# Kernel optimization log

Hardware: AMD Instinct MI355X
Metric: run time of the kernel (lower is better)

Reference implementation:

```python
import jax, jax.numpy as jnp
import numpy as np

DIM = 2048
INTER = 1408
N_EXPERTS = 16
TOP_K = 2
N_SHARED = 2
SHARED_INTER = N_SHARED * INTER  # 2816


def setup_inputs() -> dict:
    key = jax.random.key(0)
    ks = jax.random.split(key, 9)
    s = 0.02
    return {
        "x": jax.random.normal(ks[0], (4, 2048, DIM), dtype=jnp.float32),
        "gate_w": jax.random.normal(ks[1], (N_EXPERTS, DIM), dtype=jnp.float32) * s,
        "w1": jax.random.normal(ks[2], (N_EXPERTS, INTER, DIM), dtype=jnp.float32) * s,
        "w2": jax.random.normal(ks[3], (N_EXPERTS, DIM, INTER), dtype=jnp.float32) * s,
        "w3": jax.random.normal(ks[4], (N_EXPERTS, INTER, DIM), dtype=jnp.float32) * s,
        "sw1": jax.random.normal(ks[5], (SHARED_INTER, DIM), dtype=jnp.float32) * s,
        "sw2": jax.random.normal(ks[6], (DIM, SHARED_INTER), dtype=jnp.float32) * s,
        "sw3": jax.random.normal(ks[7], (SHARED_INTER, DIM), dtype=jnp.float32) * s,
    }


def _swiglu(t, wa, wb, wo):
    # t: [T, d_in]; wa, wb: [d_h, d_in]; wo: [d_out, d_h]
    h = jax.nn.silu(t @ wa.T) * (t @ wb.T)
    return h @ wo.T


def reference(x, gate_w, w1, w2, w3, sw1, sw2, sw3):
    shape = x.shape
    t = x.reshape(-1, DIM)                      # [T, dim]
    scores = jax.nn.softmax(t @ gate_w.T, axis=-1)  # [T, E]
    weights, indices = jax.lax.top_k(scores, TOP_K)  # [T, k] each

    y = jnp.zeros_like(t)
    # Small fixed loop over experts (structurally distinct weights).
    # Per-token combine weight for expert e: sum over top-k slots routed to e
    # (matches y[idx] += expert(x[idx]) * weights[idx, top]; zero weight for
    # unrouted tokens reproduces the counts[i]==0 skip exactly).
    for e in range(N_EXPERTS):
        w_e = jnp.sum(jnp.where(indices == e, weights, 0.0), axis=-1)  # [T]
        y = y + _swiglu(t, w1[e], w3[e], w2[e]) * w_e[:, None]

    z = _swiglu(t, sw1, sw3, sw2)               # shared experts MLP
    return (y + z).reshape(shape)
```

## Files before the change

kernel.cpp:

```cpp
#include <hip/hip_runtime.h>
#include <hip/hip_bf16.h>

#define DIM 2048
#define INTER 1408
#define NEXP 16
#define NTOK 8192
#define SINTER 2816

typedef __attribute__((ext_vector_type(8))) short bf16x8;
typedef __attribute__((ext_vector_type(4))) float f32x4;
typedef __attribute__((ext_vector_type(4))) unsigned short u16x4;
typedef __attribute__((ext_vector_type(8))) unsigned short u16x8;

#define VMCNT(n) asm volatile("s_waitcnt vmcnt(" #n ")" ::: "memory")
#define BARRIER() __builtin_amdgcn_s_barrier()

__device__ __forceinline__ unsigned short f2bf(float f) {
    union { float f; unsigned u; } a; a.f = f;
    unsigned r = a.u + 0x7fffu + ((a.u >> 16) & 1u);
    return (unsigned short)(r >> 16);
}

__device__ __forceinline__ void gload16(const void* g, void* lds) {
    __builtin_amdgcn_global_load_lds(
        (const __attribute__((address_space(1))) void*)g,
        (__attribute__((address_space(3))) void*)lds, 16, 0, 0);
}

__global__ __launch_bounds__(256) void cast_bf16(const float* __restrict__ s,
                                                 unsigned short* __restrict__ d,
                                                 long long n) {
    long long i = ((long long)blockIdx.x * 256 + threadIdx.x) * 8;
    if (i >= n) return;
    float4 a = *(const float4*)(s + i), b = *(const float4*)(s + i + 4);
    u16x8 o = { f2bf(a.x), f2bf(a.y), f2bf(a.z), f2bf(a.w),
                f2bf(b.x), f2bf(b.y), f2bf(b.z), f2bf(b.w) };
    *(u16x8*)(d + i) = o;
}

__global__ __launch_bounds__(256) void gate_topk(
    const float* __restrict__ x, const float* __restrict__ gw,
    unsigned short* __restrict__ xb,
    int* __restrict__ counts, int* __restrict__ toklist, float* __restrict__ tokw) {
    int wave = threadIdx.x >> 6;
    int lane = threadIdx.x & 63;
    int tok  = blockIdx.x * 4 + wave;
    const float* xr = x + (size_t)tok * DIM;
    unsigned short* xbr = xb + (size_t)tok * DIM;

    float part[NEXP];
#pragma unroll
    for (int e = 0; e < NEXP; ++e) part[e] = 0.f;
#pragma unroll
    for (int c = 0; c < DIM / 256; ++c) {
        float4 xv = *(const float4*)(xr + c * 256 + lane * 4);
        u16x4 xo = { f2bf(xv.x), f2bf(xv.y), f2bf(xv.z), f2bf(xv.w) };
        *(u16x4*)(xbr + c * 256 + lane * 4) = xo;
#pragma unroll
        for (int e = 0; e < NEXP; ++e) {
            float4 g = *(const float4*)(gw + e * DIM + c * 256 + lane * 4);
            part[e] += xv.x * g.x + xv.y * g.y + xv.z * g.z + xv.w * g.w;
        }
    }
#pragma unroll
    for (int e = 0; e < NEXP; ++e) {
        float v = part[e];
#pragma unroll
        for (int off = 32; off; off >>= 1) v += __shfl_xor(v, off);
        part[e] = v;
    }
    float mx = part[0];
#pragma unroll
    for (int e = 1; e < NEXP; ++e) mx = fmaxf(mx, part[e]);
    float Z = 0.f;
#pragma unroll
    for (int e = 0; e < NEXP; ++e) Z += expf(part[e] - mx);
    int i1 = 0; float m1 = part[0];
#pragma unroll
    for (int e = 1; e < NEXP; ++e) if (part[e] > m1) { m1 = part[e]; i1 = e; }
    int i2 = -1; float m2 = -1e30f;
#pragma unroll
    for (int e = 0; e < NEXP; ++e) if (e != i1 && part[e] > m2) { m2 = part[e]; i2 = e; }
    if (lane == 0) {
        float w1v = expf(m1 - mx) / Z;
        float w2v = expf(m2 - mx) / Z;
        int p1 = atomicAdd(&counts[i1], 1);
        toklist[i1 * NTOK + p1] = tok; tokw[i1 * NTOK + p1] = w1v;
        int p2 = atomicAdd(&counts[i2], 1);
        toklist[i2 * NTOK + p2] = tok; tokw[i2 * NTOK + p2] = w2v;
    }
}

__global__ void prefix_k(const int* __restrict__ counts, int* __restrict__ base) {
    if (threadIdx.x == 0) {
        int acc = 0;
        for (int e = 0; e < NEXP; ++e) { base[e] = acc; acc += counts[e]; }
        base[16] = acc;
        base[17] = acc + NTOK;
    }
}

__device__ __forceinline__ int swz(int r) { return (r ^ (r >> 2)) & 3; }

__global__ __launch_bounds__(512, 2) void gemm1(
    const unsigned short* __restrict__ xb,
    const unsigned short* __restrict__ w1b, const unsigned short* __restrict__ w3b,
    const unsigned short* __restrict__ sw1b, const unsigned short* __restrict__ sw3b,
    const int* __restrict__ counts, const int* __restrict__ base,
    const int* __restrict__ toklist, unsigned short* __restrict__ hbuf) {
    const int e   = blockIdx.z;
    const int cnt = (e < NEXP) ? counts[e] : NTOK;
    const int m0  = blockIdx.y * 256;
    if (m0 >= cnt) return;
    const int n0  = blockIdx.x * 128;
    const size_t woff = (size_t)((e < NEXP) ? e : e - NEXP) * INTER * DIM;
    const unsigned short* B1 = ((e < NEXP) ? w1b : sw1b) + woff;
    const unsigned short* B3 = ((e < NEXP) ? w3b : sw3b) + woff;
    const int hbase = base[e];
    const int* tl = toklist + e * NTOK;

    __shared__ __attribute__((aligned(16))) unsigned short As[4][8192];
    __shared__ __attribute__((aligned(16))) unsigned short B1s[4][4096];
    __shared__ __attribute__((aligned(16))) unsigned short B3s[4][4096];

    const int tid = threadIdx.x;
    const int w = tid >> 6, lu = tid & 63;
    const int wr = w >> 1, wc = w & 1;
    const int lr = lu & 15, hi = lu >> 4;

    const int row0 = tid >> 2, row1 = row0 + 128;
    const int c0 = (tid & 3) ^ swz(row0);
    int g0 = m0 + row0, g1 = m0 + row1;
    int t0, t1;
    if (e < NEXP) { t0 = (g0 < cnt) ? tl[g0] : 0; t1 = (g1 < cnt) ? tl[g1] : 0; }
    else          { t0 = g0; t1 = g1; }
    const unsigned short* aSrc0 = xb + (size_t)t0 * DIM + c0 * 8;
    const unsigned short* aSrc1 = xb + (size_t)t1 * DIM + c0 * 8;
    const unsigned short* b1Src = B1 + (size_t)(n0 + row0) * DIM + c0 * 8;
    const unsigned short* b3Src = B3 + (size_t)(n0 + row0) * DIM + c0 * 8;

    int aoff[4], boff[4];
#pragma unroll
    for (int m = 0; m < 4; ++m) {
        int r = wr * 64 + m * 16 + lr;
        aoff[m] = r * 64 + ((swz(r) ^ hi) << 4);
    }
#pragma unroll
    for (int n = 0; n < 4; ++n) {
        int r = wc * 64 + n * 16 + lr;
        boff[n] = r * 64 + ((swz(r) ^ hi) << 4);
    }

    f32x4 acc1[4][4], acc3[4][4];
#pragma unroll
    for (int m = 0; m < 4; ++m)
#pragma unroll
        for (int n = 0; n < 4; ++n) {
            acc1[m][n] = (f32x4){0.f, 0.f, 0.f, 0.f};
            acc3[m][n] = (f32x4){0.f, 0.f, 0.f, 0.f};
        }

    const int H = DIM / 32;

    auto STAGE = [&](int hh) {
        int hb = hh & 3;
        int kc = hh * 32;
        gload16(aSrc0 + kc, &As[hb][tid * 8]);
        gload16(aSrc1 + kc, &As[hb][4096 + tid * 8]);
        gload16(b1Src + kc, &B1s[hb][tid * 8]);
        gload16(b3Src + kc, &B3s[hb][tid * 8]);
    };

    STAGE(0); STAGE(1);
    VMCNT(4);
    BARRIER();

    for (int h = 0; h < H; ++h) {
        const int hb = h & 3;
        const char* As_ = (const char*)&As[hb][0];
        const char* B1_ = (const char*)&B1s[hb][0];
        const char* B3_ = (const char*)&B3s[hb][0];
        bf16x8 af[4], b1f[4], b3f[4];
#pragma unroll
        for (int m = 0; m < 4; ++m) af[m] = *(const bf16x8*)(As_ + aoff[m]);
#pragma unroll
        for (int n = 0; n < 4; ++n) {
            b1f[n] = *(const bf16x8*)(B1_ + boff[n]);
            b3f[n] = *(const bf16x8*)(B3_ + boff[n]);
        }
        if (h + 2 < H) { STAGE(h + 2); VMCNT(4); }
        else           { VMCNT(0); }
        BARRIER();
        __builtin_amdgcn_s_setprio(1);
#pragma unroll
        for (int n = 0; n < 4; ++n)
#pragma unroll
            for (int m = 0; m < 4; ++m)
                acc1[m][n] = __builtin_amdgcn_mfma_f32_16x16x32_bf16(af[m], b1f[n], acc1[m][n], 0, 0, 0);
#pragma unroll
        for (int n = 0; n < 4; ++n)
#pragma unroll
            for (int m = 0; m < 4; ++m)
                acc3[m][n] = __builtin_amdgcn_mfma_f32_16x16x32_bf16(af[m], b3f[n], acc3[m][n], 0, 0, 0);
        __builtin_amdgcn_s_setprio(0);
    }

#pragma unroll
    for (int m = 0; m < 4; ++m) {
#pragma unroll
        for (int i = 0; i < 4; ++i) {
            int row  = wr * 64 + m * 16 + hi * 4 + i;
            int grow = m0 + row;
            if (grow < cnt) {
                size_t ro = (size_t)(hbase + grow) * INTER;
#pragma unroll
                for (int n = 0; n < 4; ++n) {
                    int col = n0 + wc * 64 + n * 16 + lr;
                    float a = acc1[m][n][i];
                    float hv = a / (1.f + __expf(-a)) * acc3[m][n][i];
                    hbuf[ro + col] = f2bf(hv);
                }
            }
        }
    }
}

__global__ __launch_bounds__(512, 2) void gemm2(
    const unsigned short* __restrict__ hbuf,
    const unsigned short* __restrict__ w2b, const unsigned short* __restrict__ sw2b,
    const int* __restrict__ counts, const int* __restrict__ base,
    const int* __restrict__ toklist, const float* __restrict__ tokw,
    float* __restrict__ out) {
    const int e   = blockIdx.z;
    const int cnt = (e < NEXP) ? counts[e] : NTOK;
    const int m0  = blockIdx.y * 256;
    if (m0 >= cnt) return;
    const int n0  = blockIdx.x * 128;
    const int hbase = base[e];
    const size_t bstride = (e < NEXP) ? INTER : SINTER;
    const unsigned short* Bb = (e < NEXP) ? w2b + (size_t)e * DIM * INTER
                                          : sw2b + (size_t)(e - NEXP) * INTER;

    __shared__ __attribute__((aligned(16))) unsigned short Ah[4][8192];
    __shared__ __attribute__((aligned(16))) unsigned short Bh[4][4096];

    const int tid = threadIdx.x;
    const int w = tid >> 6, lu = tid & 63;
    const int wr = w >> 1, wc = w & 1;
    const int lr = lu & 15, hi = lu >> 4;

    const int row0 = tid >> 2, row1 = row0 + 128;
    const int c0 = (tid & 3) ^ swz(row0);
    const unsigned short* aSrc0 = hbuf + (size_t)(hbase + m0 + row0) * INTER + c0 * 8;
    const unsigned short* aSrc1 = hbuf + (size_t)(hbase + m0 + row1) * INTER + c0 * 8;
    const unsigned short* bSrc  = Bb + (size_t)(n0 + row0) * bstride + c0 * 8;

    int aoff[4], boff[4];
#pragma unroll
    for (int m = 0; m < 4; ++m) {
        int r = wr * 64 + m * 16 + lr;
        aoff[m] = r * 64 + ((swz(r) ^ hi) << 4);
    }
#pragma unroll
    for (int n = 0; n < 4; ++n) {
        int r = wc * 64 + n * 16 + lr;
        boff[n] = r * 64 + ((swz(r) ^ hi) << 4);
    }

    f32x4 acc[4][4];
#pragma unroll
    for (int m = 0; m < 4; ++m)
#pragma unroll
        for (int n = 0; n < 4; ++n) acc[m][n] = (f32x4){0.f, 0.f, 0.f, 0.f};

    const int H = INTER / 32;

    auto STAGE = [&](int hh) {
        int hb = hh & 3;
        int kc = hh * 32;
        gload16(aSrc0 + kc, &Ah[hb][tid * 8]);
        gload16(aSrc1 + kc, &Ah[hb][4096 + tid * 8]);
        gload16(bSrc  + kc, &Bh[hb][tid * 8]);
    };

    STAGE(0); STAGE(1);
    VMCNT(3);
    BARRIER();

    for (int h = 0; h < H; ++h) {
        const int hb = h & 3;
        const char* A_ = (const char*)&Ah[hb][0];
        const char* B_ = (const char*)&Bh[hb][0];
        bf16x8 af[4], bf[4];
#pragma unroll
        for (int m = 0; m < 4; ++m) af[m] = *(const bf16x8*)(A_ + aoff[m]);
#pragma unroll
        for (int n = 0; n < 4; ++n) bf[n] = *(const bf16x8*)(B_ + boff[n]);
        if (h + 2 < H) { STAGE(h + 2); VMCNT(3); }
        else           { VMCNT(0); }
        BARRIER();
        __builtin_amdgcn_s_setprio(1);
#pragma unroll
        for (int n = 0; n < 4; ++n)
#pragma unroll
            for (int m = 0; m < 4; ++m)
                acc[m][n] = __builtin_amdgcn_mfma_f32_16x16x32_bf16(af[m], bf[n], acc[m][n], 0, 0, 0);
        __builtin_amdgcn_s_setprio(0);
    }

#pragma unroll
    for (int m = 0; m < 4; ++m) {
#pragma unroll
        for (int i = 0; i < 4; ++i) {
            int row  = wr * 64 + m * 16 + hi * 4 + i;
            int grow = m0 + row;
            if (grow < cnt) {
                int tok; float wt;
                if (e < NEXP) { tok = toklist[e * NTOK + grow]; wt = tokw[e * NTOK + grow]; }
                else          { tok = grow; wt = 1.f; }
                float* orow = out + (size_t)tok * DIM + n0 + wc * 64 + lr;
#pragma unroll
                for (int n = 0; n < 4; ++n)
                    unsafeAtomicAdd(orow + n * 16, acc[m][n][i] * wt);
            }
        }
    }
}

extern "C" void kernel_launch(void* const* d_in, const int* in_sizes, int n_in,
                              void* d_out, int out_size, void* d_ws, size_t ws_size,
                              hipStream_t stream) {
    const float* x   = (const float*)d_in[0];
    const float* gw  = (const float*)d_in[1];
    const float* w1  = (const float*)d_in[2];
    const float* w2  = (const float*)d_in[3];
    const float* w3  = (const float*)d_in[4];
    const float* sw1 = (const float*)d_in[5];
    const float* sw2 = (const float*)d_in[6];
    const float* sw3 = (const float*)d_in[7];
    float* out = (float*)d_out;

    char* ws = (char*)d_ws;
    int*   counts  = (int*)ws;
    int*   basep   = (int*)(ws + 128);
    int*   toklist = (int*)(ws + 4096);
    float* tokw    = (float*)(ws + 4096 + (size_t)NEXP * NTOK * 4);
    unsigned short* hbuf = (unsigned short*)(ws + (2u << 20));

    const size_t hbytes = (size_t)4 * NTOK * INTER * 2;
    const size_t offx   = (2ull << 20) + hbytes;
    const size_t xbytes = (size_t)NTOK * DIM * 2;
    const size_t offw   = offx + xbytes;
    const size_t wB     = (size_t)NEXP * INTER * DIM * 2;
    const size_t swB    = (size_t)SINTER * DIM * 2;

    unsigned short* xb   = (unsigned short*)(ws + offx);
    unsigned short* w1b  = (unsigned short*)(ws + offw);
    unsigned short* w3b  = (unsigned short*)(ws + offw + wB);
    unsigned short* w2b  = (unsigned short*)(ws + offw + 2 * wB);
    unsigned short* sw1b = (unsigned short*)(ws + offw + 3 * wB);
    unsigned short* sw3b = (unsigned short*)(ws + offw + 3 * wB + swB);
    unsigned short* sw2b = (unsigned short*)(ws + offw + 3 * wB + 2 * swB);

    hipMemsetAsync(counts, 0, 64, stream);
    hipMemsetAsync(d_out, 0, (size_t)out_size * sizeof(float), stream);

    gate_topk<<<NTOK / 4, 256, 0, stream>>>(x, gw, xb, counts, toklist, tokw);
    prefix_k<<<1, 64, 0, stream>>>(counts, basep);

    auto cast = [&](const float* s, unsigned short* d, long long n) {
        cast_bf16<<<(int)((n / 8 + 255) / 256), 256, 0, stream>>>(s, d, n);
    };
    cast(w1, w1b, (long long)NEXP * INTER * DIM);
    cast(w3, w3b, (long long)NEXP * INTER * DIM);
    cast(sw1, sw1b, (long long)SINTER * DIM);
    cast(sw3, sw3b, (long long)SINTER * DIM);

    gemm1<<<dim3(INTER / 128, NTOK / 256, 18), 512, 0, stream>>>(
        xb, w1b, w3b, sw1b, sw3b, counts, basep, toklist, hbuf);

    cast(w2, w2b, (long long)NEXP * INTER * DIM);
    cast(sw2, sw2b, (long long)SINTER * DIM);

    gemm2<<<dim3(DIM / 128, NTOK / 256, 18), 512, 0, stream>>>(
        hbuf, w2b, sw2b, counts, basep, toklist, tokw, out);
}
```

Before: 1.345 ms.

## Replace atomic scatter-add output with bf16 staging buffer and combine kernel

```diff
diff --git a/kernel.cpp b/kernel.cpp
--- a/kernel.cpp
+++ b/kernel.cpp
@@ -19,6 +19,9 @@
     union { float f; unsigned u; } a; a.f = f;
     unsigned r = a.u + 0x7fffu + ((a.u >> 16) & 1u);
     return (unsigned short)(r >> 16);
+}
+__device__ __forceinline__ float bf2f(unsigned short u) {
+    union { unsigned u; float f; } a; a.u = ((unsigned)u) << 16; return a.f;
 }
 
 __device__ __forceinline__ void gload16(const void* g, void* lds) {
@@ -41,7 +44,8 @@
 __global__ __launch_bounds__(256) void gate_topk(
     const float* __restrict__ x, const float* __restrict__ gw,
     unsigned short* __restrict__ xb,
-    int* __restrict__ counts, int* __restrict__ toklist, float* __restrict__ tokw) {
+    int* __restrict__ counts, int* __restrict__ toklist,
+    int* __restrict__ se, int* __restrict__ sp, float* __restrict__ swt) {
     int wave = threadIdx.x >> 6;
     int lane = threadIdx.x & 63;
     int tok  = blockIdx.x * 4 + wave;
@@ -85,9 +89,11 @@
         float w1v = expf(m1 - mx) / Z;
         float w2v = expf(m2 - mx) / Z;
         int p1 = atomicAdd(&counts[i1], 1);
-        toklist[i1 * NTOK + p1] = tok; tokw[i1 * NTOK + p1] = w1v;
+        toklist[i1 * NTOK + p1] = tok;
         int p2 = atomicAdd(&counts[i2], 1);
-        toklist[i2 * NTOK + p2] = tok; tokw[i2 * NTOK + p2] = w2v;
+        toklist[i2 * NTOK + p2] = tok;
+        se[2 * tok] = i1;  sp[2 * tok] = p1;  swt[2 * tok] = w1v;
+        se[2 * tok + 1] = i2;  sp[2 * tok + 1] = p2;  swt[2 * tok + 1] = w2v;
     }
 }
 
@@ -229,8 +235,7 @@
     const unsigned short* __restrict__ hbuf,
     const unsigned short* __restrict__ w2b, const unsigned short* __restrict__ sw2b,
     const int* __restrict__ counts, const int* __restrict__ base,
-    const int* __restrict__ toklist, const float* __restrict__ tokw,
-    float* __restrict__ out) {
+    unsigned short* __restrict__ g2buf) {
     const int e   = blockIdx.z;
     const int cnt = (e < NEXP) ? counts[e] : NTOK;
     const int m0  = blockIdx.y * 256;
@@ -315,16 +320,38 @@
             int row  = wr * 64 + m * 16 + hi * 4 + i;
             int grow = m0 + row;
             if (grow < cnt) {
-                int tok; float wt;
-                if (e < NEXP) { tok = toklist[e * NTOK + grow]; wt = tokw[e * NTOK + grow]; }
-                else          { tok = grow; wt = 1.f; }
-                float* orow = out + (size_t)tok * DIM + n0 + wc * 64 + lr;
+                unsigned short* orow = g2buf + (size_t)(hbase + grow) * DIM + n0 + wc * 64 + lr;
 #pragma unroll
                 for (int n = 0; n < 4; ++n)
-                    unsafeAtomicAdd(orow + n * 16, acc[m][n][i] * wt);
+                    orow[n * 16] = f2bf(acc[m][n][i]);
             }
         }
     }
+}
+
+__global__ __launch_bounds__(256) void combine(
+    const unsigned short* __restrict__ g2buf, const int* __restrict__ base,
+    const int* __restrict__ se, const int* __restrict__ sp,
+    const float* __restrict__ swt, float* __restrict__ out) {
+    const int tok = blockIdx.x;
+    const int c = threadIdx.x * 8;
+    const int e0 = se[2 * tok], e1 = se[2 * tok + 1];
+    const float w0 = swt[2 * tok], w1 = swt[2 * tok + 1];
+    const size_t r0 = (size_t)(base[e0] + sp[2 * tok]) * DIM + c;
+    const size_t r1 = (size_t)(base[e1] + sp[2 * tok + 1]) * DIM + c;
+    const size_t r2 = (size_t)(2 * NTOK + tok) * DIM + c;
+    const size_t r3 = (size_t)(3 * NTOK + tok) * DIM + c;
+    u16x8 a = *(const u16x8*)(g2buf + r0);
+    u16x8 b = *(const u16x8*)(g2buf + r1);
+    u16x8 s0 = *(const u16x8*)(g2buf + r2);
+    u16x8 s1 = *(const u16x8*)(g2buf + r3);
+    float o[8];
+#pragma unroll
+    for (int j = 0; j < 8; ++j)
+        o[j] = w0 * bf2f(a[j]) + w1 * bf2f(b[j]) + bf2f(s0[j]) + bf2f(s1[j]);
+    float4* op = (float4*)(out + (size_t)tok * DIM + c);
+    op[0] = make_float4(o[0], o[1], o[2], o[3]);
+    op[1] = make_float4(o[4], o[5], o[6], o[7]);
 }
 
 extern "C" void kernel_launch(void* const* d_in, const int* in_sizes, int n_in,
@@ -344,7 +371,14 @@
     int*   counts  = (int*)ws;
     int*   basep   = (int*)(ws + 128);
     int*   toklist = (int*)(ws + 4096);
-    float* tokw    = (float*)(ws + 4096 + (size_t)NEXP * NTOK * 4);
+    int*   se      = (int*)(ws + 4096 + (5 << 19));
+    int*   sp      = (int*)(ws + 4096 + (5 << 19) + (1 << 16));
+    float* swt     = (float*)(ws + 4096 + (5 << 19) + (2 << 16));
+
+    se  = (int*)(ws + 4096 + 524288);
+    sp  = (int*)(ws + 4096 + 524288 + 65536);
+    swt = (float*)(ws + 4096 + 524288 + 131072);
+
     unsigned short* hbuf = (unsigned short*)(ws + (2u << 20));
 
     const size_t hbytes = (size_t)4 * NTOK * INTER * 2;
@@ -362,10 +396,11 @@
     unsigned short* sw3b = (unsigned short*)(ws + offw + 3 * wB + swB);
     unsigned short* sw2b = (unsigned short*)(ws + offw + 3 * wB + 2 * swB);
 
+    unsigned short* g2buf = (unsigned short*)(ws + offx);
+
     hipMemsetAsync(counts, 0, 64, stream);
-    hipMemsetAsync(d_out, 0, (size_t)out_size * sizeof(float), stream);
-
-    gate_topk<<<NTOK / 4, 256, 0, stream>>>(x, gw, xb, counts, toklist, tokw);
+
+    gate_topk<<<NTOK / 4, 256, 0, stream>>>(x, gw, xb, counts, toklist, se, sp, swt);
     prefix_k<<<1, 64, 0, stream>>>(counts, basep);
 
     auto cast = [&](const float* s, unsigned short* d, long long n) {
@@ -383,5 +418,7 @@
     cast(sw2, sw2b, (long long)SINTER * DIM);
 
     gemm2<<<dim3(DIM / 128, NTOK / 256, 18), 512, 0, stream>>>(
-        hbuf, w2b, sw2b, counts, basep, toklist, tokw, out);
-}
+        hbuf, w2b, sw2b, counts, basep, g2buf);
+
+    combine<<<NTOK, 256, 0, stream>>>(g2buf, basep, se, sp, swt, out);
+}
```

Result: faster. 1.278 ms (-5.0%).
